# Optimization experiments

Measured on AMD Instinct MI355X. Metric: run time of the kernel, lower is better.

## Reference

```python
import jax, jax.numpy as jnp
import numpy as np

_SAMPLING_EPS = 1e-5
BIG_NEG = jnp.float32(-1e30)  # finite stand-in for -inf (exact 0 after softmax in fp32)


def setup_inputs() -> dict:
    key = jax.random.key(0)
    ks = jax.random.split(key, 12)
    B, V, P, O, S = 128, 128000, 2048, 256, 4
    return {
        "logits": jax.random.normal(ks[0], (B, V), jnp.float32) * 4.0,
        "prompt_token_ids": jax.random.randint(ks[1], (B, P), 0, V),
        "output_token_ids": jax.random.randint(ks[2], (B, O), 0, V),
        "stop_token_ids": jax.random.randint(ks[3], (B, S), 0, V),
        "min_tokens": jax.random.randint(ks[4], (B,), 0, 512),
        "presence_penalties": jax.random.uniform(ks[5], (B,), jnp.float32),
        "frequency_penalties": jax.random.uniform(ks[6], (B,), jnp.float32),
        "repetition_penalties": 1.0 + 0.3 * jax.random.uniform(ks[7], (B,), jnp.float32),
        "temperature": 0.5 + jax.random.uniform(ks[8], (B,), jnp.float32),
        "top_k": jax.random.randint(ks[9], (B,), 32, 64),
        "top_p": 0.5 + 0.5 * jax.random.uniform(ks[10], (B,), jnp.float32),
        "uniform_noise": jax.random.uniform(ks[11], (B, V), jnp.float32, minval=1e-10, maxval=1.0),
        "max_num_logprobs": 20,
    }


def reference(logits, prompt_token_ids, output_token_ids, stop_token_ids,
              min_tokens, presence_penalties, frequency_penalties,
              repetition_penalties, temperature, top_k, top_p,
              uniform_noise, max_num_logprobs):
    B, V = logits.shape
    x = logits.astype(jnp.float32)
    rows = jnp.arange(B)[:, None]

    # ---- min-token penalty: set stop-token logits to -inf while len(output) < min_tokens
    need = min_tokens > output_token_ids.shape[1]                  # [B]
    stop_pen = jnp.where(need[:, None], BIG_NEG, jnp.inf)          # [B,S]
    x = x.at[rows, stop_token_ids].min(stop_pen)

    # ---- presence / frequency / repetition penalties (vLLM apply_penalties)
    counts = jnp.zeros((B, V), jnp.float32).at[rows, output_token_ids].add(1.0)
    prompt_mask = jnp.zeros((B, V), bool).at[rows, prompt_token_ids].set(True)
    output_mask = counts > 0
    rp = repetition_penalties[:, None]
    penalized = jnp.where(x > 0, x / rp, x * rp)
    x = jnp.where(prompt_mask | output_mask, penalized, x)
    x = x - frequency_penalties[:, None] * counts \
          - presence_penalties[:, None] * output_mask.astype(jnp.float32)

    # ---- temperature (greedy rows: temp treated as 1.0)
    t = jnp.where(temperature < _SAMPLING_EPS, 1.0, temperature)
    x = x / t[:, None]

    # ---- top-k / top-p filtering (per-row k and p)
    order = jnp.argsort(-x, axis=-1)                               # descending
    srt = jnp.take_along_axis(x, order, axis=-1)
    pos = jnp.arange(V)[None, :]
    k_eff = jnp.where(top_k < 1, V, top_k)
    keep_k = pos < k_eff[:, None]
    probs_s = jax.nn.softmax(srt, axis=-1)
    cum = jnp.cumsum(probs_s, axis=-1)
    keep_p = (cum - probs_s) < top_p[:, None]                      # cumulative mass before token < p
    keep = jnp.zeros((B, V), bool).at[rows, order].set(keep_k & keep_p)
    x = jnp.where(keep, x, BIG_NEG)

    orig_logits = x
    # source applies temperature a second time before the final sample
    x2 = x / t[:, None]

    # ---- sample: Gumbel-max random sampling, greedy where temperature ~ 0
    gumbel = -jnp.log(-jnp.log(uniform_noise))
    random_sampled = jnp.argmax(x2 + gumbel, axis=-1)
    greedy_sampled = jnp.argmax(x2, axis=-1)
    sampled = jnp.where(temperature < _SAMPLING_EPS, greedy_sampled,
                        random_sampled).astype(jnp.int32)

    # ---- top-k logprobs
    logprobs = jax.nn.log_softmax(orig_logits, axis=-1)
    topk_logprobs, topk_indices = jax.lax.top_k(logprobs, max_num_logprobs)
    return sampled, topk_logprobs, topk_indices.astype(jnp.int32)
```

## Files before the change

kernel.cpp:

```cpp
#include <hip/hip_runtime.h>
#include <math.h>

#define VV 128000
#define NB 128
#define PP 2048
#define OO 256

#define S   8
#define CH  16000
#define CW  500
#define NT1 512
#define CAP 512
#define HS1 512

#define NT2 256

#define BIG_NEG_F (-1e30f)
#define PAD_KEY 0x007FFFFF80000000ULL
#define LOG2E 1.4426950408889634f

__device__ __forceinline__ unsigned long long packkey(float f, int idx) {
  unsigned int b = __float_as_uint(f);
  unsigned int mf = (b & 0x80000000u) ? ~b : (b | 0x80000000u);
  return ((unsigned long long)mf << 32) | (unsigned long long)(unsigned int)(~(unsigned int)idx);
}
__device__ __forceinline__ float unpack_val(unsigned long long k) {
  unsigned int mf = (unsigned int)(k >> 32);
  unsigned int b = (mf & 0x80000000u) ? (mf & 0x7fffffffu) : ~mf;
  return __uint_as_float(b);
}
__device__ __forceinline__ int unpack_idx(unsigned long long k) {
  return (int)(~(unsigned int)(k & 0xffffffffu));
}

__device__ __forceinline__ float wave_sort64_desc(float v, int lane) {
  for (int k = 2; k <= 64; k <<= 1) {
    for (int j = k >> 1; j > 0; j >>= 1) {
      float o = __shfl_xor(v, j, 64);
      bool smaller = (lane & j) == 0;
      bool dir = (lane & k) == 0;
      v = (smaller == dir) ? fmaxf(v, o) : fminf(v, o);
    }
  }
  return v;
}
__device__ __forceinline__ unsigned long long wave_sort64_desc_u64(unsigned long long v, int lane) {
  for (int k = 2; k <= 64; k <<= 1) {
    for (int j = k >> 1; j > 0; j >>= 1) {
      unsigned long long o = __shfl_xor(v, j, 64);
      bool smaller = (lane & j) == 0;
      bool dir = (lane & k) == 0;
      unsigned long long mx = (v > o) ? v : o;
      unsigned long long mn = (v > o) ? o : v;
      v = (smaller == dir) ? mx : mn;
    }
  }
  return v;
}
__device__ __forceinline__ unsigned long long merge_top64(unsigned long long v,
                                                          const unsigned long long* B,
                                                          int lane) {
  unsigned long long b = B[63 - lane];
  v = (v > b) ? v : b;
  for (int j = 32; j > 0; j >>= 1) {
    unsigned long long o = __shfl_xor(v, j, 64);
    bool hi = (lane & j) == 0;
    unsigned long long mx = (v > o) ? v : o;
    unsigned long long mn = (v > o) ? o : v;
    v = hi ? mx : mn;
  }
  return v;
}

__global__ __launch_bounds__(NT1, 4)
void k_main(const float* __restrict__ logits,
            const int* __restrict__ prompt_ids,
            const int* __restrict__ output_ids,
            const int* __restrict__ stop_ids,
            const int* __restrict__ min_tokens,
            const float* __restrict__ presence_p,
            const float* __restrict__ frequency_p,
            const float* __restrict__ repetition_p,
            const float* __restrict__ temperature,
            float* __restrict__ ws_sum,
            unsigned long long* __restrict__ ws_top)
{
#pragma clang fp contract(off)
  __shared__ uint2 masks[CW];
  __shared__ int hkey[HS1];
  __shared__ int hval[HS1];
  __shared__ unsigned long long cand[CAP];
  __shared__ unsigned long long mbuf[4 * 64];
  __shared__ float wtau[NT1 / 64];
  __shared__ float wsum[NT1 / 64];
  __shared__ float tau_sh;
  __shared__ int cnt_sh;

  const int chunk = blockIdx.x;
  const int row   = blockIdx.y;
  const int tid   = threadIdx.x;
  const int lane  = tid & 63;
  const int wv    = tid >> 6;
  const int base  = chunk * CH;

  const float fp  = frequency_p[row];
  const float pp  = presence_p[row];
  const float rp  = repetition_p[row];
  const float inv_rp = 1.0f / rp;
  const float tmp = temperature[row];
  const float t   = (tmp < 1e-5f) ? 1.0f : tmp;
  const float c2  = LOG2E / t;
  const bool need = min_tokens[row] > OO;
  const int s0 = stop_ids[row * 4 + 0];
  const int s1 = stop_ids[row * 4 + 1];
  const int s2 = stop_ids[row * 4 + 2];
  const int s3 = stop_ids[row * 4 + 3];
  const bool anystop = need &&
      (((unsigned)(s0 - base) < CH) || ((unsigned)(s1 - base) < CH) ||
       ((unsigned)(s2 - base) < CH) || ((unsigned)(s3 - base) < CH));

  const int4 tv = ((const int4*)(prompt_ids + (size_t)row * PP))[tid];
  const bool havetok = tid < OO;
  int tok = 0;
  if (havetok) tok = output_ids[row * OO + tid];

  for (int i = tid; i < CW; i += NT1) { masks[i].x = 0u; masks[i].y = 0u; }
  for (int i = tid; i < HS1; i += NT1) { hkey[i] = -1; hval[i] = 0; }
  if (tid == 0) cnt_sh = 0;
  __syncthreads();

  {
    int l;
    l = tv.x - base; if ((unsigned)l < CH) atomicOr(&masks[l >> 5].x, 1u << (l & 31));
    l = tv.y - base; if ((unsigned)l < CH) atomicOr(&masks[l >> 5].x, 1u << (l & 31));
    l = tv.z - base; if ((unsigned)l < CH) atomicOr(&masks[l >> 5].x, 1u << (l & 31));
    l = tv.w - base; if ((unsigned)l < CH) atomicOr(&masks[l >> 5].x, 1u << (l & 31));
  }
  if (havetok) {
    int l = tok - base;
    if ((unsigned)l < CH) {
      atomicOr(&masks[l >> 5].y, 1u << (l & 31));
      unsigned int h = ((unsigned int)tok * 2654435761u) >> 23;
      for (;;) {
        int k = hkey[h];
        if (k == tok) { atomicAdd(&hval[h], 1); break; }
        if (k == -1) {
          int prev = atomicCAS(&hkey[h], -1, tok);
          if (prev == -1 || prev == tok) { atomicAdd(&hval[h], 1); break; }
          continue;
        }
        h = (h + 1) & (HS1 - 1);
      }
    }
  }

  unsigned int stopmask = 0u;
  if (anystop) {
    const int sids[4] = {s0, s1, s2, s3};
#pragma unroll
    for (int q = 0; q < 4; ++q) {
      int local = sids[q] - base;
      if ((unsigned)local < CH) {
        int grp = (local >> 3) / NT1;
        int tt  = (local >> 3) % NT1;
        if (tt == tid) stopmask |= 1u << (grp * 8 + (local & 7));
      }
    }
  }
  __syncthreads();

  const float* __restrict__ lrow = logits + (size_t)row * VV + base;
  const int l0 = (0 * NT1 + tid) << 3;
  const int l1 = (1 * NT1 + tid) << 3;
  const int l2 = (2 * NT1 + tid) << 3;
  const int l3 = (3 * NT1 + tid) << 3;
  const bool v3 = l3 < CH;

  float4 A0 = *(const float4*)(lrow + l0);
  float4 B0 = *(const float4*)(lrow + l0 + 4);
  float4 A1 = *(const float4*)(lrow + l1);
  float4 B1 = *(const float4*)(lrow + l1 + 4);
  float4 A2 = *(const float4*)(lrow + l2);
  float4 B2 = *(const float4*)(lrow + l2 + 4);
  float4 A3, B3;
  if (v3) { A3 = *(const float4*)(lrow + l3); B3 = *(const float4*)(lrow + l3 + 4); }

  float px0[8], px1[8], px2[8], px3[8];
  float gm0 = -INFINITY, gm1 = -INFINITY, gm2 = -INFINITY, gm3 = -INFINITY;
  float esum = 0.0f;

  auto processA = [&](int li, float4 xa, float4 xb, float (&px)[8],
                      float& gm, unsigned int sm8) {
    unsigned int w  = (unsigned)li >> 5;
    unsigned int sh = (unsigned)li & 31u;
    uint2 mw = masks[w];
    unsigned int pm8 = (mw.x >> sh) & 255u;
    unsigned int om8 = (mw.y >> sh) & 255u;
    float xs[8] = {xa.x, xa.y, xa.z, xa.w, xb.x, xb.y, xb.z, xb.w};
    if (sm8) {
#pragma unroll
      for (int e = 0; e < 8; ++e)
        if ((sm8 >> e) & 1u) xs[e] = BIG_NEG_F;
    }
#pragma unroll
    for (int e = 0; e < 8; ++e) {
      float xp = xs[e];
      float xe = xp;
      if ((pm8 | om8) & (1u << e)) {
        float xa_ = (xp > 0.0f) ? (xp * inv_rp) : (xp * rp);
        float xd_ = (xp > 0.0f) ? (xp / rp)     : (xp * rp);
        if ((om8 >> e) & 1u) {
          int v = base + li + e;
          float cnt = 0.0f;
          unsigned int h = ((unsigned int)v * 2654435761u) >> 23;
          for (;;) {
            int k = hkey[h];
            if (k == -1) break;
            if (k == v) { cnt = (float)hval[h]; break; }
            h = (h + 1) & (HS1 - 1);
          }
          xa_ = xa_ - fp * cnt - pp;
          xd_ = xd_ - fp * cnt - pp;
        }
        esum += exp2f(xa_ * c2);
        xe = xd_;
      } else {
        esum += exp2f(xp * c2);
      }
      gm = fmaxf(gm, xe);
      px[e] = xe;
    }
  };

  processA(l0, A0, B0, px0, gm0, stopmask & 255u);
  processA(l1, A1, B1, px1, gm1, (stopmask >> 8) & 255u);
  processA(l2, A2, B2, px2, gm2, (stopmask >> 16) & 255u);
  if (v3) processA(l3, A3, B3, px3, gm3, (stopmask >> 24) & 255u);

  float mx = fmaxf(fmaxf(gm0, gm1), fmaxf(gm2, gm3));

  float ss = esum;
#pragma unroll
  for (int off = 32; off > 0; off >>= 1) ss += __shfl_down(ss, off, 64);
  if (lane == 0) wsum[wv] = ss;

  float srt = wave_sort64_desc(mx, lane);
  if (lane == 7) wtau[wv] = srt;
  __syncthreads();

  if (tid == 0) {
    float tau = wtau[0];
#pragma unroll
    for (int w = 1; w < NT1 / 64; ++w) tau = fminf(tau, wtau[w]);
    tau_sh = tau;
    float sacc = 0.0f;
#pragma unroll
    for (int w = 0; w < NT1 / 64; ++w) sacc += wsum[w];
    ws_sum[row * S + chunk] = sacc;
  }
  __syncthreads();
  const float taueff = tau_sh;

  auto processB = [&](int li, const float (&px)[8], float gmv) {
    if (gmv < taueff) return;
#pragma unroll
    for (int e = 0; e < 8; ++e) {
      float xe = px[e];
      if (xe >= taueff) {
        float xd = xe / t;
        int p = atomicAdd(&cnt_sh, 1);
        if (p < CAP) cand[p] = packkey(xd, base + li + e);
      }
    }
  };

  processB(l0, px0, gm0);
  processB(l1, px1, gm1);
  processB(l2, px2, gm2);
  if (v3) processB(l3, px3, gm3);

  __syncthreads();
  int total = cnt_sh; if (total > CAP) total = CAP;
  int runs = (total + 63) >> 6; if (runs < 1) runs = 1;
  const int tree = (runs <= 1) ? 1 : (runs == 2) ? 2 : (runs <= 4) ? 4 : 8;
  const int padto = tree << 6;
  for (int i = tid; i < padto; i += NT1)
    if (i >= total) cand[i] = PAD_KEY;
  __syncthreads();

  if (wv < runs) {
    unsigned long long rv = wave_sort64_desc_u64(cand[(wv << 6) + lane], lane);
    cand[(wv << 6) + lane] = rv;
  }
  __syncthreads();

  unsigned long long* outp = &ws_top[((size_t)row * S + chunk) * 64 + lane];
  if (tree == 8) {
    if (wv < 4) {
      unsigned long long a = cand[((2 * wv) << 6) + lane];
      a = merge_top64(a, &cand[(2 * wv + 1) << 6], lane);
      mbuf[(wv << 6) + lane] = a;
    }
    __syncthreads();
    if (wv < 2) {
      unsigned long long a = mbuf[((2 * wv) << 6) + lane];
      a = merge_top64(a, &mbuf[(2 * wv + 1) << 6], lane);
      cand[(wv << 6) + lane] = a;
    }
    __syncthreads();
    if (wv == 0) {
      unsigned long long a = cand[lane];
      a = merge_top64(a, &cand[64], lane);
      *outp = a;
    }
  } else if (tree == 4) {
    if (wv < 2) {
      unsigned long long a = cand[((2 * wv) << 6) + lane];
      a = merge_top64(a, &cand[(2 * wv + 1) << 6], lane);
      mbuf[(wv << 6) + lane] = a;
    }
    __syncthreads();
    if (wv == 0) {
      unsigned long long a = mbuf[lane];
      a = merge_top64(a, &mbuf[64], lane);
      *outp = a;
    }
  } else if (tree == 2) {
    if (wv == 0) {
      unsigned long long a = cand[lane];
      a = merge_top64(a, &cand[64], lane);
      *outp = a;
    }
  } else {
    if (wv == 0) *outp = cand[lane];
  }
}

__global__ __launch_bounds__(NT2)
void k2_finalize(const float* __restrict__ temperature,
                 const int* __restrict__ top_k,
                 const float* __restrict__ top_p,
                 const float* __restrict__ noise,
                 const unsigned long long* __restrict__ ws_top,
                 const float* __restrict__ ws_sum,
                 float* __restrict__ out, int K)
{
#pragma clang fp contract(off)
  __shared__ unsigned long long buf[S * 64];
  __shared__ unsigned long long mbuf[4 * 64];
  __shared__ float ssh[S];
  __shared__ float sv[64];
  __shared__ int   si[64];
  __shared__ float se[64];
  __shared__ float rr[64];

  const int row  = blockIdx.x;
  const int tid  = threadIdx.x;
  const int lane = tid & 63;
  const int wv   = tid >> 6;

  const float tmp = temperature[row];
  const float t   = (tmp < 1e-5f) ? 1.0f : tmp;
  const int   tk  = top_k[row];
  const float tpv = top_p[row];

  if (tid < S) ssh[tid] = ws_sum[row * S + tid];
  for (int i = tid; i < S * 64; i += NT2)
    buf[i] = ws_top[(size_t)row * S * 64 + i];
  __syncthreads();

  {
    unsigned long long a = buf[((2 * wv) << 6) + lane];
    a = merge_top64(a, &buf[(2 * wv + 1) << 6], lane);
    mbuf[(wv << 6) + lane] = a;
  }
  __syncthreads();
  if (wv < 2) {
    unsigned long long a = mbuf[((2 * wv) << 6) + lane];
    a = merge_top64(a, &mbuf[(2 * wv + 1) << 6], lane);
    buf[(wv << 6) + lane] = a;
  }
  __syncthreads();
  if (wv != 0) return;

  unsigned long long a = buf[lane];
  a = merge_top64(a, &buf[64], lane);
  float val = unpack_val(a);
  int   idx = unpack_idx(a);
  float m = __shfl(val, 0, 64);
  sv[lane] = val;
  si[lane] = idx;
  bool ok = (unsigned)idx < VV;
  float u = ok ? noise[(size_t)row * VV + idx] : 0.5f;
  float g = -logf(-logf(u));
  float sej = expf(val - m);
  se[lane] = sej;
  float gvv = val / t + g;

  float Ssum = 0.0f;
#pragma unroll
  for (int c = 0; c < S; ++c) Ssum += ssh[c];
  const float Z = Ssum * exp2f(-m * LOG2E);
  rr[lane] = sej / Z;

  int keff = (tk < 1) ? 64 : (tk < 64 ? tk : 64);
  float cum = 0.0f;
  int nk = 0;
  for (int j = 0; j < 64; j++) {
    if (j >= keff) break;
    if (!(cum < tpv)) break;
    nk++;
    cum += rr[j];
  }

  float cv = (lane < nk) ? gvv : -INFINITY;
  int   ci = (lane < nk) ? idx : 0x7fffffff;
#pragma unroll
  for (int off = 32; off > 0; off >>= 1) {
    float ov = __shfl_xor(cv, off, 64);
    int   oi = __shfl_xor(ci, off, 64);
    if (ov > cv || (ov == cv && oi < ci)) { cv = ov; ci = oi; }
  }

  if (lane == 0) {
    float Zk = 0.0f;
    for (int j = 0; j < nk; j++) Zk += se[j];
    const float logZk = logf(Zk);

    const int samp = (tmp < 1e-5f) ? si[0] : ci;
    out[row] = (float)samp;

    unsigned long long bm0 = 0ull, bm1 = 0ull;
    for (int j = 0; j < nk; j++) {
      int ix = si[j];
      if (ix < 64) bm0 |= 1ull << ix;
      else if (ix < 128) bm1 |= 1ull << (ix - 64);
    }
    int fi = 0;
    for (int j = 0; j < K; j++) {
      float lp; int ix;
      if (j < nk) {
        lp = (sv[j] - m) - logZk;
        ix = si[j];
      } else {
        while ((fi < 64) ? ((bm0 >> fi) & 1ull) : ((bm1 >> (fi - 64)) & 1ull)) fi++;
        ix = fi; fi++;
        lp = BIG_NEG_F;
      }
      out[NB + row * K + j]            = lp;
      out[NB + NB * K + row * K + j]   = (float)ix;
    }
  }
}

extern "C" void kernel_launch(void* const* d_in, const int* in_sizes, int n_in,
                              void* d_out, int out_size, void* d_ws, size_t ws_size,
                              hipStream_t stream) {
  const float* logits = (const float*)d_in[0];
  const int*   prompt = (const int*)d_in[1];
  const int*   outids = (const int*)d_in[2];
  const int*   stop   = (const int*)d_in[3];
  const int*   mint   = (const int*)d_in[4];
  const float* pres   = (const float*)d_in[5];
  const float* freq   = (const float*)d_in[6];
  const float* rep    = (const float*)d_in[7];
  const float* temp   = (const float*)d_in[8];
  const int*   topk   = (const int*)d_in[9];
  const float* topp   = (const float*)d_in[10];
  const float* noise  = (const float*)d_in[11];

  int B_ = in_sizes[4];
  int K_ = (out_size - B_) / (2 * B_);

  float* ws_sum = (float*)d_ws;
  unsigned long long* ws_top = (unsigned long long*)(ws_sum + (size_t)NB * S);

  dim3 g1(S, B_);
  k_main<<<g1, NT1, 0, stream>>>(logits, prompt, outids, stop, mint,
                                 pres, freq, rep, temp, ws_sum, ws_top);
  k2_finalize<<<B_, NT2, 0, stream>>>(temp, topk, topp, noise,
                                      ws_top, ws_sum, (float*)d_out, K_);
}
```

Before: 185.0 us.

## Split each row into 16 chunks instead of 8 and deepen finalize merge tree

Doubles the number of per-row chunks in the first kernel (S 8→16, CH 16000→8000), so each block processes half as many logits. Each thread now handles two 8-element groups instead of four. The grid gets twice as many blocks, for more parallelism and latency hiding on the large GPU. In exchange, the finalize kernel gets an extra merge level over 16 top-64 lists, and there is twice the per-chunk overhead: mask building, sorting and writing to the workspace.

```diff
diff --git a/kernel.cpp b/kernel.cpp
--- a/kernel.cpp
+++ b/kernel.cpp
@@ -6,9 +6,9 @@
 #define PP 2048
 #define OO 256
 
-#define S   8
-#define CH  16000
-#define CW  500
+#define S   16
+#define CH  8000
+#define CW  250
 #define NT1 512
 #define CAP 512
 #define HS1 512
@@ -172,21 +172,15 @@
   const float* __restrict__ lrow = logits + (size_t)row * VV + base;
   const int l0 = (0 * NT1 + tid) << 3;
   const int l1 = (1 * NT1 + tid) << 3;
-  const int l2 = (2 * NT1 + tid) << 3;
-  const int l3 = (3 * NT1 + tid) << 3;
-  const bool v3 = l3 < CH;
+  const bool v1 = l1 < CH;
 
   float4 A0 = *(const float4*)(lrow + l0);
   float4 B0 = *(const float4*)(lrow + l0 + 4);
-  float4 A1 = *(const float4*)(lrow + l1);
-  float4 B1 = *(const float4*)(lrow + l1 + 4);
-  float4 A2 = *(const float4*)(lrow + l2);
-  float4 B2 = *(const float4*)(lrow + l2 + 4);
-  float4 A3, B3;
-  if (v3) { A3 = *(const float4*)(lrow + l3); B3 = *(const float4*)(lrow + l3 + 4); }
-
-  float px0[8], px1[8], px2[8], px3[8];
-  float gm0 = -INFINITY, gm1 = -INFINITY, gm2 = -INFINITY, gm3 = -INFINITY;
+  float4 A1, B1;
+  if (v1) { A1 = *(const float4*)(lrow + l1); B1 = *(const float4*)(lrow + l1 + 4); }
+
+  float px0[8], px1[8];
+  float gm0 = -INFINITY, gm1 = -INFINITY;
   float esum = 0.0f;
 
   auto processA = [&](int li, float4 xa, float4 xb, float (&px)[8],
@@ -233,11 +227,9 @@
   };
 
   processA(l0, A0, B0, px0, gm0, stopmask & 255u);
-  processA(l1, A1, B1, px1, gm1, (stopmask >> 8) & 255u);
-  processA(l2, A2, B2, px2, gm2, (stopmask >> 16) & 255u);
-  if (v3) processA(l3, A3, B3, px3, gm3, (stopmask >> 24) & 255u);
-
-  float mx = fmaxf(fmaxf(gm0, gm1), fmaxf(gm2, gm3));
+  if (v1) processA(l1, A1, B1, px1, gm1, (stopmask >> 8) & 255u);
+
+  float mx = fmaxf(gm0, gm1);
 
   float ss = esum;
 #pragma unroll
@@ -275,9 +267,7 @@
   };
 
   processB(l0, px0, gm0);
-  processB(l1, px1, gm1);
-  processB(l2, px2, gm2);
-  if (v3) processB(l3, px3, gm3);
+  if (v1) processB(l1, px1, gm1);
 
   __syncthreads();
   int total = cnt_sh; if (total > CAP) total = CAP;
@@ -347,7 +337,7 @@
 {
 #pragma clang fp contract(off)
   __shared__ unsigned long long buf[S * 64];
-  __shared__ unsigned long long mbuf[4 * 64];
+  __shared__ unsigned long long mbuf[8 * 64];
   __shared__ float ssh[S];
   __shared__ float sv[64];
   __shared__ int   si[64];
@@ -369,22 +359,29 @@
     buf[i] = ws_top[(size_t)row * S * 64 + i];
   __syncthreads();
 
+#pragma unroll
+  for (int r = wv; r < 8; r += 4) {
+    unsigned long long a = buf[((2 * r) << 6) + lane];
+    a = merge_top64(a, &buf[(2 * r + 1) << 6], lane);
+    mbuf[(r << 6) + lane] = a;
+  }
+  __syncthreads();
   {
+    unsigned long long a = mbuf[((2 * wv) << 6) + lane];
+    a = merge_top64(a, &mbuf[(2 * wv + 1) << 6], lane);
+    buf[(wv << 6) + lane] = a;
+  }
+  __syncthreads();
+  if (wv < 2) {
     unsigned long long a = buf[((2 * wv) << 6) + lane];
     a = merge_top64(a, &buf[(2 * wv + 1) << 6], lane);
     mbuf[(wv << 6) + lane] = a;
   }
   __syncthreads();
-  if (wv < 2) {
-    unsigned long long a = mbuf[((2 * wv) << 6) + lane];
-    a = merge_top64(a, &mbuf[(2 * wv + 1) << 6], lane);
-    buf[(wv << 6) + lane] = a;
-  }
-  __syncthreads();
   if (wv != 0) return;
 
-  unsigned long long a = buf[lane];
-  a = merge_top64(a, &buf[64], lane);
+  unsigned long long a = mbuf[lane];
+  a = merge_top64(a, &mbuf[64], lane);
   float val = unpack_val(a);
   int   idx = unpack_idx(a);
   float m = __shfl(val, 0, 64);
```

After: 182.4 us. Within noise of the previous version (-1.4%).
